# Optimization experiments

Measured on AMD Instinct MI355X. Metric: run time of the kernel, lower is better.

The kernel has to match this reference:

```python
import jax, jax.numpy as jnp
import numpy as np

CNT_R = 500
DIM = 128
B, NEI = 8192, 64


def setup_inputs() -> dict:
    key = jax.random.key(0)
    ks = jax.random.split(key, 10)
    d2 = 2 * DIM
    return {
        "batch_nei_e_emb": jax.random.normal(ks[0], (B, NEI, DIM), dtype=jnp.float32),
        "batch_nei_rw": jax.random.uniform(ks[1], (B, NEI), dtype=jnp.float32),
        "w_r_table": jax.random.normal(ks[2], (2 * CNT_R + 1, DIM), dtype=jnp.float32),
        "zq_table": jax.random.normal(ks[3], (2 * CNT_R, DIM), dtype=jnp.float32),
        "attn_W_w": jax.random.normal(ks[4], (d2, d2), dtype=jnp.float32) / np.sqrt(d2),
        "attn_W_b": jnp.zeros((d2,), dtype=jnp.float32),
        "u_a_w": jax.random.normal(ks[5], (d2,), dtype=jnp.float32) / np.sqrt(d2),
        "u_a_b": jnp.zeros((), dtype=jnp.float32),
        "batch_nei_rid": jax.random.randint(ks[6], (B, NEI), 0, 2 * CNT_R + 1),
        "batch_q_rid": jax.random.randint(ks[7], (B,), 0, 2 * CNT_R),
    }


def reference(batch_nei_e_emb, batch_nei_rw, w_r_table, zq_table,
              attn_W_w, attn_W_b, u_a_w, u_a_b,
              batch_nei_rid, batch_q_rid):
    # gather relation hyperplane normals: (B, NEI, DIM)
    w_r = w_r_table[batch_nei_rid]
    n = w_r / jnp.linalg.norm(w_r, axis=-1, keepdims=True)
    # hyperplane projection: e - (e . n) n
    e = batch_nei_e_emb
    e_proj = e - jnp.sum(e * n, axis=-1, keepdims=True) * n
    # query relation embedding, tiled over neighbors: (B, NEI, DIM)
    z_q = zq_table[batch_q_rid]  # (B, DIM)
    z_q = jnp.broadcast_to(z_q[:, None, :], e_proj.shape)
    concat = jnp.concatenate([z_q, e_proj], axis=-1)  # (B, NEI, 2*DIM)
    h = jnp.tanh(jnp.einsum('bni,oi->bno', concat, attn_W_w) + attn_W_b)
    _alpha = jnp.einsum('bni,i->bn', h, u_a_w) + u_a_b  # (B, NEI)
    alpha = jax.nn.softmax(_alpha, axis=-1)
    attn = alpha + batch_nei_rw
    return attn
```

## Files before the change

kernel.cpp:

```cpp
#include <hip/hip_runtime.h>
#include <hip/hip_bf16.h>

#define NB    8192
#define NEI   64
#define DIM   128
#define D2    256
#define NR_W  1001
#define NR_Z  1000
#define EPB_LD 136
#define BPB   16
#define C2L2E 2.8853900817779268f

typedef __attribute__((ext_vector_type(8))) short bf16x8;
typedef __attribute__((ext_vector_type(4))) float f32x4;

__device__ __forceinline__ ushort f2bf(float x) {
    union { float f; unsigned u; } c; c.f = x;
    unsigned u = c.u;
    return (ushort)((u + 0x7fffu + ((u >> 16) & 1u)) >> 16);
}

__device__ __forceinline__ unsigned pk2(float a, float b) {
    __hip_bfloat162 h = __float22bfloat162_rn(make_float2(a, b));
    return *(unsigned*)&h;
}

__device__ __forceinline__ void gll16(const void* g, void* l) {
    __builtin_amdgcn_global_load_lds(
        (const __attribute__((address_space(1))) unsigned int*)g,
        (__attribute__((address_space(3))) unsigned int*)l, 16, 0, 0);
}


__global__ void k_norm(const float* __restrict__ w_r_table, float* __restrict__ norm_t) {
    int r = blockIdx.x;
    int t = threadIdx.x;
    float v = w_r_table[r * DIM + t];
    float s = v * v;
    #pragma unroll
    for (int m = 1; m < 64; m <<= 1) s += __shfl_xor(s, m);
    __shared__ float sh[2];
    if ((t & 63) == 0) sh[t >> 6] = s;
    __syncthreads();
    float tot = sh[0] + sh[1];
    norm_t[r * DIM + t] = v / sqrtf(tot);
}

__global__ void k_tq(const float* __restrict__ zq_table, const float* __restrict__ W,
                     const float* __restrict__ bias, float* __restrict__ tq_t) {
    int r = blockIdx.x;
    int o = threadIdx.x;
    __shared__ float4 z4[32];
    if (o < 32) z4[o] = ((const float4*)(zq_table + r * DIM))[o];
    __syncthreads();
    const float4* wr = (const float4*)(W + o * D2);
    float acc = bias[o];
    #pragma unroll 8
    for (int i = 0; i < 32; ++i) {
        float4 wv = wr[i], zv = z4[i];
        acc += wv.x*zv.x + wv.y*zv.y + wv.z*zv.z + wv.w*zv.w;
    }
    tq_t[r * D2 + o] = acc;
}

__global__ void k_bfrag(const float* __restrict__ W, ushort* __restrict__ bfrag) {
    int ot = blockIdx.x;
    int kt = blockIdx.y;
    int l  = threadIdx.x;
    int o  = ot * 16 + (l & 15);
    int k  = kt * 32 + (l >> 4) * 8;
    const float4* src = (const float4*)(W + o * D2 + DIM + k);
    float4 a = src[0], c = src[1];
    uint4 w;
    w.x = f2bf(a.x) | ((unsigned)f2bf(a.y) << 16);
    w.y = f2bf(a.z) | ((unsigned)f2bf(a.w) << 16);
    w.z = f2bf(c.x) | ((unsigned)f2bf(c.y) << 16);
    w.w = f2bf(c.z) | ((unsigned)f2bf(c.w) << 16);
    *(uint4*)(bfrag + ((ot * 4 + kt) * 64 + l) * 8) = w;
}

__global__ void k_sua(const float* __restrict__ u, float* __restrict__ sua) {
    int t = threadIdx.x;
    float v = u[t];
    #pragma unroll
    for (int m = 1; m < 64; m <<= 1) v += __shfl_xor(v, m);
    __shared__ float sh[4];
    if ((t & 63) == 0) sh[t >> 6] = v;
    __syncthreads();
    if (t == 0) sua[0] = sh[0] + sh[1] + sh[2] + sh[3];
}


__global__ __launch_bounds__(512, 4) void k_main(
    const float* __restrict__ e_emb,
    const float* __restrict__ rw,
    const int*   __restrict__ nei_rid,
    const int*   __restrict__ q_rid,
    const float* __restrict__ norm_t,
    const float* __restrict__ tq_t,
    const ushort* __restrict__ bfrag,
    const float* __restrict__ u_a_sum,
    const float* __restrict__ u_a_w,
    float* __restrict__ out)
{
    __shared__ __align__(16) float  e_raw[NEI * DIM];
    __shared__ __align__(16) ushort ep16[NEI * EPB_LD];
    __shared__ float alpw[8][NEI];

    const int t    = threadIdx.x;
    const int wave = t >> 6, lane = t & 63;
    const int ln   = lane & 15, hi = lane >> 4;
    const int row  = t >> 3, q3 = t & 7;
    const int b0   = blockIdx.x * BPB;

    bf16x8 bfr_[2][4];
    #pragma unroll
    for (int nt = 0; nt < 2; ++nt)
        #pragma unroll
        for (int kt = 0; kt < 4; ++kt)
            bfr_[nt][kt] = *(const bf16x8*)(bfrag + ((((wave*2+nt)*4 + kt)*64 + lane)*8));
    asm volatile("" : "+v"(bfr_[0][0]), "+v"(bfr_[0][1]), "+v"(bfr_[0][2]), "+v"(bfr_[0][3]),
                      "+v"(bfr_[1][0]), "+v"(bfr_[1][1]), "+v"(bfr_[1][2]), "+v"(bfr_[1][3]));

    float ua2[2];
    #pragma unroll
    for (int nt = 0; nt < 2; ++nt) ua2[nt] = u_a_w[wave*32 + nt*16 + ln];
    asm volatile("" : "+v"(ua2[0]), "+v"(ua2[1]));
    const float sua = u_a_sum[0];

    unsigned soff[4];
    #pragma unroll
    for (int c = 0; c < 4; ++c) {
        unsigned D = (unsigned)(wave*4096 + c*1024 + lane*16);
        unsigned r7 = (unsigned)((wave*8 + 2*c + (lane>>5)) & 7);
        soff[c] = D ^ (r7 << 4);
    }
    const char* ebase = (const char*)e_emb;

    #pragma unroll
    for (int c = 0; c < 4; ++c)
        gll16(ebase + (((size_t)b0) << 15) + soff[c], (char*)e_raw + wave*4096 + c*1024);
    int   rid_c = nei_rid[b0 * NEI + row];
    float rw_c  = rw[(size_t)b0 * NEI + (t & 63)];
    float tqc[2];
    {
        int qr = q_rid[b0];
        #pragma unroll
        for (int nt = 0; nt < 2; ++nt)
            tqc[nt] = C2L2E * tq_t[qr * D2 + wave*32 + nt*16 + ln];
    }
    int   rid_n = 0;  float rw_n = 0.f;  float tqn[2] = {0.f, 0.f};

    __syncthreads();

    #pragma unroll 1
    for (int i = 0; i < BPB; ++i) {
        const int b = b0 + i;

        {
            const float4* nsrc = (const float4*)(norm_t + rid_c * DIM + q3 * 16);
            float4 nv[4];
            #pragma unroll
            for (int k = 0; k < 4; ++k) nv[k] = nsrc[k];
            const unsigned rbase = (unsigned)(row * 512 + q3 * 64);
            const unsigned rx = (unsigned)((row & 7) << 4);
            float4 ev[4];
            #pragma unroll
            for (int k = 0; k < 4; ++k)
                ev[k] = *(const float4*)((const char*)e_raw + ((rbase + k*16) ^ rx));
            float part = 0.f;
            #pragma unroll
            for (int k = 0; k < 4; ++k)
                part += ev[k].x*nv[k].x + ev[k].y*nv[k].y + ev[k].z*nv[k].z + ev[k].w*nv[k].w;
            part += __shfl_xor(part, 1);
            part += __shfl_xor(part, 2);
            part += __shfl_xor(part, 4);
            const float d = part;
            float p0 = fmaf(-d, nv[0].x, ev[0].x), p1 = fmaf(-d, nv[0].y, ev[0].y);
            float p2 = fmaf(-d, nv[0].z, ev[0].z), p3 = fmaf(-d, nv[0].w, ev[0].w);
            float p4 = fmaf(-d, nv[1].x, ev[1].x), p5 = fmaf(-d, nv[1].y, ev[1].y);
            float p6 = fmaf(-d, nv[1].z, ev[1].z), p7 = fmaf(-d, nv[1].w, ev[1].w);
            uint4 w0; w0.x = pk2(p0,p1); w0.y = pk2(p2,p3); w0.z = pk2(p4,p5); w0.w = pk2(p6,p7);
            float s0 = fmaf(-d, nv[2].x, ev[2].x), s1 = fmaf(-d, nv[2].y, ev[2].y);
            float s2 = fmaf(-d, nv[2].z, ev[2].z), s3 = fmaf(-d, nv[2].w, ev[2].w);
            float s4 = fmaf(-d, nv[3].x, ev[3].x), s5 = fmaf(-d, nv[3].y, ev[3].y);
            float s6 = fmaf(-d, nv[3].z, ev[3].z), s7 = fmaf(-d, nv[3].w, ev[3].w);
            uint4 w1; w1.x = pk2(s0,s1); w1.y = pk2(s2,s3); w1.z = pk2(s4,s5); w1.w = pk2(s6,s7);
            char* dst = (char*)ep16 + row * (EPB_LD*2) + q3 * 32;
            *(uint4*)dst = w0;
            *(uint4*)(dst + 16) = w1;
        }

        __syncthreads();

        if (i + 1 < BPB) {
            const size_t ebo = ((size_t)(b + 1)) << 15;
            #pragma unroll
            for (int c = 0; c < 4; ++c)
                gll16(ebase + ebo + soff[c], (char*)e_raw + wave*4096 + c*1024);
            rid_n = nei_rid[(b + 1) * NEI + row];
            rw_n  = rw[(size_t)(b + 1) * NEI + (t & 63)];
            int qr1 = q_rid[b + 1];
            #pragma unroll
            for (int nt = 0; nt < 2; ++nt)
                tqn[nt] = tq_t[qr1 * D2 + wave*32 + nt*16 + ln];
        }

        #pragma unroll
        for (int mt = 0; mt < 4; ++mt) {
            bf16x8 a_[4];
            #pragma unroll
            for (int kt = 0; kt < 4; ++kt)
                a_[kt] = *(const bf16x8*)&ep16[(mt*16 + ln) * EPB_LD + kt*32 + hi*8];
            f32x4 acc[2];
            #pragma unroll
            for (int nt = 0; nt < 2; ++nt) acc[nt] = (f32x4){0.f, 0.f, 0.f, 0.f};
            #pragma unroll
            for (int kt = 0; kt < 4; ++kt)
                #pragma unroll
                for (int nt = 0; nt < 2; ++nt)
                    acc[nt] = __builtin_amdgcn_mfma_f32_16x16x32_bf16(a_[kt], bfr_[nt][kt], acc[nt], 0, 0, 0);
            float pr[4] = {0.f, 0.f, 0.f, 0.f};
            #pragma unroll
            for (int nt = 0; nt < 2; ++nt)
                #pragma unroll
                for (int j = 0; j < 4; ++j) {
                    float e2 = __builtin_exp2f(fmaf(C2L2E, acc[nt][j], tqc[nt]));
                    float r  = __builtin_amdgcn_rcpf(e2 + 1.f);
                    pr[j] = fmaf(ua2[nt], r, pr[j]);
                }
            #pragma unroll
            for (int m = 1; m < 16; m <<= 1)
                #pragma unroll
                for (int j = 0; j < 4; ++j) pr[j] += __shfl_xor(pr[j], m);
            if (ln == 0) {
                #pragma unroll
                for (int j = 0; j < 4; ++j) alpw[wave][mt*16 + hi*4 + j] = pr[j];
            }
        }

        __syncthreads();

        if (t < NEI) {
            float s8 = 0.f;
            #pragma unroll
            for (int w = 0; w < 8; ++w) s8 += alpw[w][t];
            float a = fmaf(-2.f, s8, sua);
            float p = __expf(a);
            float s = p;
            #pragma unroll
            for (int m = 1; m < 64; m <<= 1) s += __shfl_xor(s, m);
            out[(size_t)b * NEI + t] = fmaf(p, __builtin_amdgcn_rcpf(s), rw_c);
        }

        if (i + 1 < BPB) {
            rid_c = rid_n;
            rw_c  = rw_n;
            tqc[0] = C2L2E * tqn[0];
            tqc[1] = C2L2E * tqn[1];
            asm volatile("" : "+v"(rid_c), "+v"(rw_c), "+v"(tqc[0]), "+v"(tqc[1]));
        }
    }
}


extern "C" void kernel_launch(void* const* d_in, const int* in_sizes, int n_in,
                              void* d_out, int out_size, void* d_ws, size_t ws_size,
                              hipStream_t stream) {
    const float* e_emb   = (const float*)d_in[0];
    const float* rw      = (const float*)d_in[1];
    const float* w_r_tab = (const float*)d_in[2];
    const float* zq_tab  = (const float*)d_in[3];
    const float* attn_W  = (const float*)d_in[4];
    const float* attn_b  = (const float*)d_in[5];
    const float* u_a_w   = (const float*)d_in[6];
    const int*   nei_rid = (const int*)d_in[8];
    const int*   q_rid   = (const int*)d_in[9];
    float* out = (float*)d_out;

    float* ws = (float*)d_ws;
    float* norm_t = ws;
    float* tq_t   = norm_t + NR_W * DIM;
    ushort* bfrag = (ushort*)(tq_t + NR_Z * D2);
    float* suap   = (float*)(bfrag + 16*4*64*8);

    k_norm<<<NR_W, DIM, 0, stream>>>(w_r_tab, norm_t);
    k_tq<<<NR_Z, D2, 0, stream>>>(zq_tab, attn_W, attn_b, tq_t);
    k_bfrag<<<dim3(16, 4), 64, 0, stream>>>(attn_W, bfrag);
    k_sua<<<1, 256, 0, stream>>>(u_a_w, suap);
    k_main<<<NB / BPB, 512, 0, stream>>>(e_emb, rw, nei_rid, q_rid,
                                         norm_t, tq_t, bfrag, suap, u_a_w, out);
}
```

Measured before the change: 151.2 us.

## Drop LDS staging and prefetch pipeline; load embeddings directly with smaller batches per block

Removes the async global-to-LDS prefetch of the next batch's embeddings and the register double-buffering of rid/rw/tq. Each thread now reads embeddings and normals straight from global memory, and batches per block drop from 16 to 2, so the grid gets larger. This frees 32KB of LDS per block, which can raise occupancy, and relies on more resident waves to hide latency instead of explicit software pipelining. The cost is losing the overlap of loads with MFMA work and paying more per-block setup, such as reloading the B fragments.

```diff
diff --git a/kernel.cpp b/kernel.cpp
--- a/kernel.cpp
+++ b/kernel.cpp
@@ -8,7 +8,7 @@
 #define NR_W  1001
 #define NR_Z  1000
 #define EPB_LD 136
-#define BPB   16
+#define BPB   2
 #define C2L2E 2.8853900817779268f
 
 typedef __attribute__((ext_vector_type(8))) short bf16x8;
@@ -23,12 +23,6 @@
 __device__ __forceinline__ unsigned pk2(float a, float b) {
     __hip_bfloat162 h = __float22bfloat162_rn(make_float2(a, b));
     return *(unsigned*)&h;
-}
-
-__device__ __forceinline__ void gll16(const void* g, void* l) {
-    __builtin_amdgcn_global_load_lds(
-        (const __attribute__((address_space(1))) unsigned int*)g,
-        (__attribute__((address_space(3))) unsigned int*)l, 16, 0, 0);
 }
 
 
@@ -103,7 +97,6 @@
     const float* __restrict__ u_a_w,
     float* __restrict__ out)
 {
-    __shared__ __align__(16) float  e_raw[NEI * DIM];
     __shared__ __align__(16) ushort ep16[NEI * EPB_LD];
     __shared__ float alpw[8][NEI];
 
@@ -121,90 +114,54 @@
             bfr_[nt][kt] = *(const bf16x8*)(bfrag + ((((wave*2+nt)*4 + kt)*64 + lane)*8));
     asm volatile("" : "+v"(bfr_[0][0]), "+v"(bfr_[0][1]), "+v"(bfr_[0][2]), "+v"(bfr_[0][3]),
                       "+v"(bfr_[1][0]), "+v"(bfr_[1][1]), "+v"(bfr_[1][2]), "+v"(bfr_[1][3]));
-
     float ua2[2];
     #pragma unroll
     for (int nt = 0; nt < 2; ++nt) ua2[nt] = u_a_w[wave*32 + nt*16 + ln];
     asm volatile("" : "+v"(ua2[0]), "+v"(ua2[1]));
     const float sua = u_a_sum[0];
 
-    unsigned soff[4];
-    #pragma unroll
-    for (int c = 0; c < 4; ++c) {
-        unsigned D = (unsigned)(wave*4096 + c*1024 + lane*16);
-        unsigned r7 = (unsigned)((wave*8 + 2*c + (lane>>5)) & 7);
-        soff[c] = D ^ (r7 << 4);
-    }
-    const char* ebase = (const char*)e_emb;
-
-    #pragma unroll
-    for (int c = 0; c < 4; ++c)
-        gll16(ebase + (((size_t)b0) << 15) + soff[c], (char*)e_raw + wave*4096 + c*1024);
-    int   rid_c = nei_rid[b0 * NEI + row];
-    float rw_c  = rw[(size_t)b0 * NEI + (t & 63)];
-    float tqc[2];
-    {
-        int qr = q_rid[b0];
-        #pragma unroll
-        for (int nt = 0; nt < 2; ++nt)
-            tqc[nt] = C2L2E * tq_t[qr * D2 + wave*32 + nt*16 + ln];
-    }
-    int   rid_n = 0;  float rw_n = 0.f;  float tqn[2] = {0.f, 0.f};
-
-    __syncthreads();
-
     #pragma unroll 1
     for (int i = 0; i < BPB; ++i) {
         const int b = b0 + i;
 
         {
-            const float4* nsrc = (const float4*)(norm_t + rid_c * DIM + q3 * 16);
-            float4 nv[4];
-            #pragma unroll
-            for (int k = 0; k < 4; ++k) nv[k] = nsrc[k];
-            const unsigned rbase = (unsigned)(row * 512 + q3 * 64);
-            const unsigned rx = (unsigned)((row & 7) << 4);
-            float4 ev[4];
-            #pragma unroll
-            for (int k = 0; k < 4; ++k)
-                ev[k] = *(const float4*)((const char*)e_raw + ((rbase + k*16) ^ rx));
+            const int rid = nei_rid[b * NEI + row];
+            const float4* esrc = (const float4*)(e_emb + ((size_t)b * NEI + row) * DIM);
+            const float4* nsrc = (const float4*)(norm_t + rid * DIM);
+            float4 ev[4], nv[4];
+            #pragma unroll
+            for (int kk = 0; kk < 4; ++kk) {
+                ev[kk] = esrc[q3 + 8*kk];
+                nv[kk] = nsrc[q3 + 8*kk];
+            }
             float part = 0.f;
             #pragma unroll
-            for (int k = 0; k < 4; ++k)
-                part += ev[k].x*nv[k].x + ev[k].y*nv[k].y + ev[k].z*nv[k].z + ev[k].w*nv[k].w;
+            for (int kk = 0; kk < 4; ++kk)
+                part += ev[kk].x*nv[kk].x + ev[kk].y*nv[kk].y + ev[kk].z*nv[kk].z + ev[kk].w*nv[kk].w;
             part += __shfl_xor(part, 1);
             part += __shfl_xor(part, 2);
             part += __shfl_xor(part, 4);
             const float d = part;
-            float p0 = fmaf(-d, nv[0].x, ev[0].x), p1 = fmaf(-d, nv[0].y, ev[0].y);
-            float p2 = fmaf(-d, nv[0].z, ev[0].z), p3 = fmaf(-d, nv[0].w, ev[0].w);
-            float p4 = fmaf(-d, nv[1].x, ev[1].x), p5 = fmaf(-d, nv[1].y, ev[1].y);
-            float p6 = fmaf(-d, nv[1].z, ev[1].z), p7 = fmaf(-d, nv[1].w, ev[1].w);
-            uint4 w0; w0.x = pk2(p0,p1); w0.y = pk2(p2,p3); w0.z = pk2(p4,p5); w0.w = pk2(p6,p7);
-            float s0 = fmaf(-d, nv[2].x, ev[2].x), s1 = fmaf(-d, nv[2].y, ev[2].y);
-            float s2 = fmaf(-d, nv[2].z, ev[2].z), s3 = fmaf(-d, nv[2].w, ev[2].w);
-            float s4 = fmaf(-d, nv[3].x, ev[3].x), s5 = fmaf(-d, nv[3].y, ev[3].y);
-            float s6 = fmaf(-d, nv[3].z, ev[3].z), s7 = fmaf(-d, nv[3].w, ev[3].w);
-            uint4 w1; w1.x = pk2(s0,s1); w1.y = pk2(s2,s3); w1.z = pk2(s4,s5); w1.w = pk2(s6,s7);
-            char* dst = (char*)ep16 + row * (EPB_LD*2) + q3 * 32;
-            *(uint4*)dst = w0;
-            *(uint4*)(dst + 16) = w1;
+            #pragma unroll
+            for (int kk = 0; kk < 4; ++kk) {
+                float p0 = fmaf(-d, nv[kk].x, ev[kk].x);
+                float p1 = fmaf(-d, nv[kk].y, ev[kk].y);
+                float p2 = fmaf(-d, nv[kk].z, ev[kk].z);
+                float p3 = fmaf(-d, nv[kk].w, ev[kk].w);
+                uint2 w2; w2.x = pk2(p0, p1); w2.y = pk2(p2, p3);
+                *(uint2*)((char*)ep16 + row * (EPB_LD*2) + (q3 + 8*kk) * 8) = w2;
+            }
+        }
+
+        float tq2[2];
+        {
+            int qr = q_rid[b];
+            #pragma unroll
+            for (int nt = 0; nt < 2; ++nt)
+                tq2[nt] = C2L2E * tq_t[qr * D2 + wave*32 + nt*16 + ln];
         }
 
         __syncthreads();
-
-        if (i + 1 < BPB) {
-            const size_t ebo = ((size_t)(b + 1)) << 15;
-            #pragma unroll
-            for (int c = 0; c < 4; ++c)
-                gll16(ebase + ebo + soff[c], (char*)e_raw + wave*4096 + c*1024);
-            rid_n = nei_rid[(b + 1) * NEI + row];
-            rw_n  = rw[(size_t)(b + 1) * NEI + (t & 63)];
-            int qr1 = q_rid[b + 1];
-            #pragma unroll
-            for (int nt = 0; nt < 2; ++nt)
-                tqn[nt] = tq_t[qr1 * D2 + wave*32 + nt*16 + ln];
-        }
 
         #pragma unroll
         for (int mt = 0; mt < 4; ++mt) {
@@ -225,7 +182,7 @@
             for (int nt = 0; nt < 2; ++nt)
                 #pragma unroll
                 for (int j = 0; j < 4; ++j) {
-                    float e2 = __builtin_exp2f(fmaf(C2L2E, acc[nt][j], tqc[nt]));
+                    float e2 = __builtin_exp2f(fmaf(C2L2E, acc[nt][j], tq2[nt]));
                     float r  = __builtin_amdgcn_rcpf(e2 + 1.f);
                     pr[j] = fmaf(ua2[nt], r, pr[j]);
                 }
@@ -250,15 +207,7 @@
             float s = p;
             #pragma unroll
             for (int m = 1; m < 64; m <<= 1) s += __shfl_xor(s, m);
-            out[(size_t)b * NEI + t] = fmaf(p, __builtin_amdgcn_rcpf(s), rw_c);
-        }
-
-        if (i + 1 < BPB) {
-            rid_c = rid_n;
-            rw_c  = rw_n;
-            tqc[0] = C2L2E * tqn[0];
-            tqc[1] = C2L2E * tqn[1];
-            asm volatile("" : "+v"(rid_c), "+v"(rw_c), "+v"(tqc[0]), "+v"(tqc[1]));
+            out[(size_t)b * NEI + t] = fmaf(p, __builtin_amdgcn_rcpf(s), rw[(size_t)b * NEI + t]);
         }
     }
 }
```

New measurement: 143.7 us. 4.9% less time.
